# Performance work log

Measured on AMD Instinct MI355X. Metric: run time of the kernel, lower is better.

Reference implementation:

```python
import jax, jax.numpy as jnp
import numpy as np

N = 131072   # total inner-graph nodes (G * n)
G = 2048     # number of inner graphs = nodes of outer graph fg
n = 64       # nodes per inner graph (contiguous blocks)
E = 1048576  # inner edges
EF = 32768   # outer (fg) edges
D = 128      # emb_dim == hidden_dim
K = 8        # SortPooling k
VOCAB = 150


def setup_inputs() -> dict:
    key = jax.random.key(0)
    ks = jax.random.split(key, 32)
    p = lambda k, shape: (jax.random.normal(k, shape, jnp.float32) * 0.1)
    inp = {
        'h': jax.random.randint(ks[0], (N,), 0, VOCAB),
        'g_src': jax.random.randint(ks[1], (E,), 0, N),
        'g_dst': jax.random.randint(ks[2], (E,), 0, N),
        'fg_src': jax.random.randint(ks[3], (EF,), 0, G),
        'fg_dst': jax.random.randint(ks[4], (EF,), 0, G),
        'token_emb': p(ks[5], (VOCAB, D)),
        # GATConv 1 (D -> D, 1 head): fc weight (in,out), attn vectors, output bias
        'W1': p(ks[6], (D, D)), 'al1': p(ks[7], (D,)), 'ar1': p(ks[8], (D,)), 'b1': p(ks[9], (D,)),
        # GATConv 2
        'W2': p(ks[10], (D, D)), 'al2': p(ks[11], (D,)), 'ar2': p(ks[12], (D,)), 'b2': p(ks[13], (D,)),
        # GATConv 3 (K*D -> D) over fg
        'W3': p(ks[14], (K * D, D)), 'al3': p(ks[15], (D,)), 'ar3': p(ks[16], (D,)), 'b3': p(ks[17], (D,)),
        # linear_forward
        'Wf': p(ks[18], (D, D)), 'bf': p(ks[19], (D,)),
        # linear
        'Wl': p(ks[20], (D, D)), 'bl': p(ks[21], (D,)),
        # linear1
        'Wl1': p(ks[22], (D, D)), 'bl1': p(ks[23], (D,)),
        # clasifier
        'Wc': p(ks[24], (D, 2)), 'bc': p(ks[25], (2,)),
    }
    return inp


def gat_conv(src, dst, num_nodes, x, W, al, ar, b):
    """DGL GATConv, num_heads=1, allow_zero_in_degree=True, no activation."""
    f = x @ W                                   # [N, D] projected features
    el = f @ al                                 # [N] left attention logits
    er = f @ ar                                 # [N] right attention logits
    e = jax.nn.leaky_relu(el[src] + er[dst], 0.2)   # [E] per-edge score
    m = jax.ops.segment_max(e, dst, num_segments=num_nodes)
    a = jnp.exp(e - m[dst])
    s = jax.ops.segment_sum(a, dst, num_segments=num_nodes)
    alpha = a / s[dst]                          # edge softmax over incoming edges
    out = jax.ops.segment_sum(alpha[:, None] * f[src], dst, num_segments=num_nodes)
    return out + b                              # zero-in-degree nodes -> bias only


def sort_pooling(x, num_graphs, nodes_per_graph, k):
    """DGL SortPooling: sort each node's feature ascending, rank nodes by last
    channel descending, take top-k, concat -> [G, k*D]."""
    d = x.shape[-1]
    x = jnp.sort(x.reshape(num_graphs, nodes_per_graph, d), axis=-1)
    idx = jnp.argsort(-x[:, :, -1], axis=1)[:, :k]          # [G, k]
    topk = jnp.take_along_axis(x, idx[:, :, None], axis=1)  # [G, k, D]
    return topk.reshape(num_graphs, k * d)


def reference(h, g_src, g_dst, fg_src, fg_dst, token_emb,
              W1, al1, ar1, b1, W2, al2, ar2, b2, W3, al3, ar3, b3,
              Wf, bf, Wl, bl, Wl1, bl1, Wc, bc):
    x = jax.nn.relu(token_emb[h])                                   # [N, D]
    x = jax.nn.relu(gat_conv(g_src, g_dst, N, x, W1, al1, ar1, b1))
    x = jax.nn.relu(gat_conv(g_src, g_dst, N, x, W2, al2, ar2, b2))
    x = jax.nn.relu(x @ Wf + bf)                                    # linear_forward
    x = sort_pooling(x, G, n, K)                                    # [G, K*D]
    x = jax.nn.relu(gat_conv(fg_src, fg_dst, G, x, W3, al3, ar3, b3))
    x = jax.nn.relu(x @ Wl + bl)                                    # dropout = eval identity
    x = jax.nn.relu(x @ Wl1 + bl1)
    x = x @ Wc + bc
    return x.reshape(-1, 2)
```

## Files before the change

### kernel.cpp

```cpp
#include <hip/hip_runtime.h>
#include <math.h>

#define NN   131072
#define GG   2048
#define NPG  64
#define EE   1048576
#define EFN  32768
#define DD   128
#define KK   8
#define VOCAB 150

typedef unsigned short bfu;
typedef _Float16 f16x8 __attribute__((ext_vector_type(8)));
typedef float f32x4 __attribute__((ext_vector_type(4)));

static __device__ __forceinline__ bfu f2b(float f) {
  unsigned u = __float_as_uint(f);
  u += 0x7FFFu + ((u >> 16) & 1u);
  return (bfu)(u >> 16);
}
static __device__ __forceinline__ float b2f(bfu b) {
  return __uint_as_float(((unsigned)b) << 16);
}

static __device__ __forceinline__ bfu f2h(float f) {
  _Float16 h = (_Float16)f;
  bfu u;
  __builtin_memcpy(&u, &h, 2);
  return u;
}
static __device__ __forceinline__ float h2f(bfu b) {
  _Float16 h;
  __builtin_memcpy(&h, &b, 2);
  return (float)h;
}

__global__ void fill_f32_kernel(float* __restrict__ p, float v, int nElems) {
  int i = blockIdx.x * 256 + threadIdx.x;
  if (i < nElems) p[i] = v;
}

__global__ void zero_int_kernel(int* __restrict__ p, int nElems) {
  int i = blockIdx.x * 256 + threadIdx.x;
  if (i < nElems) p[i] = 0;
}

__global__ void init_softmax_kernel(float* __restrict__ mx, float* __restrict__ sm, int nElems) {
  int i = blockIdx.x * 256 + threadIdx.x;
  if (i < nElems) { mx[i] = -INFINITY; sm[i] = 0.f; }
}

__global__ void embed_relu_kernel(const float* __restrict__ temb,
                                  const int* __restrict__ h,
                                  float* __restrict__ x, int total) {
  int i = blockIdx.x * 256 + threadIdx.x;
  if (i >= total) return;
  int node = i >> 7, d = i & 127;
  x[i] = fmaxf(temb[h[node] * DD + d], 0.f);
}

template <int KD, int ROWS>
__global__ __launch_bounds__(128) void gemm_kernel(
    const float* __restrict__ A, const float* __restrict__ W,
    const float* __restrict__ bias, float* __restrict__ out,
    int relu_flag) {
  __shared__ float As[ROWS * KD];
  const int row0 = blockIdx.x * ROWS;
  const int tid = threadIdx.x;
  for (int i = tid; i < ROWS * KD; i += 128) As[i] = A[(size_t)row0 * KD + i];
  __syncthreads();
  float acc[ROWS];
#pragma unroll
  for (int r = 0; r < ROWS; r++) acc[r] = 0.f;
  for (int k = 0; k < KD; k++) {
    float w = W[k * 128 + tid];
#pragma unroll
    for (int r = 0; r < ROWS; r++) acc[r] += As[r * KD + k] * w;
  }
  float b = bias ? bias[tid] : 0.f;
#pragma unroll
  for (int r = 0; r < ROWS; r++) {
    float v = acc[r] + b;
    if (relu_flag) v = fmaxf(v, 0.f);
    out[(size_t)(row0 + r) * 128 + tid] = v;
  }
}

__global__ __launch_bounds__(128) void vocab_l1_kernel(
    const float* __restrict__ temb, const float* __restrict__ W1,
    const float* __restrict__ al1, const float* __restrict__ ar1,
    bfu* __restrict__ fvh, float* __restrict__ elv, float* __restrict__ erv) {
  __shared__ float xs[128];
  __shared__ float rl[128], rr[128];
  int v = blockIdx.x, t = threadIdx.x;
  xs[t] = fmaxf(temb[v * 128 + t], 0.f);
  __syncthreads();
  float acc = 0.f;
  for (int k = 0; k < 128; k++) acc += xs[k] * W1[k * 128 + t];
  fvh[v * 128 + t] = f2h(acc);
  rl[t] = acc * al1[t];
  rr[t] = acc * ar1[t];
  __syncthreads();
  for (int off = 64; off; off >>= 1) {
    if (t < off) { rl[t] += rl[t + off]; rr[t] += rr[t + off]; }
    __syncthreads();
  }
  if (t == 0) { elv[v] = rl[0]; erv[v] = rr[0]; }
}

__global__ __launch_bounds__(256) void gemm1024_kernel(
    const float* __restrict__ A, const float* __restrict__ W,
    float* __restrict__ out,
    const float* __restrict__ al, const float* __restrict__ ar,
    float* __restrict__ el, float* __restrict__ er) {
  __shared__ float As[8 * 1024];
  __shared__ float red[8][256];
  const int t = threadIdx.x;
  const int row0 = blockIdx.x * 8;
  for (int idx = t; idx < 8 * 256; idx += 256) {
    int r = idx >> 8, c4 = (idx & 255) << 2;
    *(float4*)&As[r * 1024 + c4] = *(const float4*)(A + (size_t)(row0 + r) * 1024 + c4);
  }
  __syncthreads();
  const int col = t & 127, kh = t >> 7;
  const int k0 = kh * 512;
  float acc[8];
#pragma unroll
  for (int r = 0; r < 8; r++) acc[r] = 0.f;
  for (int k = k0; k < k0 + 512; k += 4) {
    float w0 = W[(size_t)(k + 0) * 128 + col];
    float w1 = W[(size_t)(k + 1) * 128 + col];
    float w2 = W[(size_t)(k + 2) * 128 + col];
    float w3 = W[(size_t)(k + 3) * 128 + col];
#pragma unroll
    for (int r = 0; r < 8; r++) {
      float4 a = *(const float4*)&As[r * 1024 + k];
      acc[r] += a.x * w0 + a.y * w1 + a.z * w2 + a.w * w3;
    }
  }
#pragma unroll
  for (int r = 0; r < 8; r++) red[r][t] = acc[r];
  __syncthreads();
  for (int idx = t; idx < 1024; idx += 256) {
    int r = idx >> 7, c = idx & 127;
    float val = red[r][c] + red[r][128 + c];
    out[(size_t)(row0 + r) * 128 + c] = val;
    As[idx] = val * al[c];
    As[4096 + idx] = val * ar[c];
  }
  __syncthreads();
  if (t < 8) {
    float s = 0.f;
    for (int c = 0; c < 128; c++) s += As[t * 128 + c];
    el[row0 + t] = s;
  } else if (t < 16) {
    int r = t - 8;
    float s = 0.f;
    for (int c = 0; c < 128; c++) s += As[4096 + r * 128 + c];
    er[row0 + r] = s;
  }
}

__global__ void pack_w2_kernel(const float* __restrict__ W2, const float* __restrict__ Wf,
                               bfu* __restrict__ w2h, bfu* __restrict__ wfh) {
  int i = blockIdx.x * 256 + threadIdx.x;
  if (i >= 32768) return;
  const float* W = (i < 16384) ? W2 : Wf;
  bfu* dst = (i < 16384) ? w2h : wfh;
  int ii = i & 16383;
  int k = ii >> 7, n = ii & 127;
  bfu h = f2h(W[ii]);
  int kk = k >> 5, k5 = k & 31, quad = k5 >> 3, j = k5 & 7;
  int tt = n >> 4, m16 = n & 15;
  int pos = ((((kk * 8 + tt) * 4 + quad) * 16) + m16) * 8 + j;
  dst[pos] = h;
}

template <int SRC_MODE, int EPI>
__global__ __launch_bounds__(256) void mfma_gemm(
    const float* A, const bfu* __restrict__ WfHi,
    const float* __restrict__ bias, void* out,
    const float* __restrict__ al, const float* __restrict__ ar,
    float* __restrict__ el, float* __restrict__ er,
    float* __restrict__ keyb) {
  const int t = threadIdx.x;
  const int lane = t & 63, wv_ = t >> 6;
  const int m16 = lane & 15, quad = lane >> 4;
  const int rowbase = blockIdx.x * 128 + wv_ * 32;
  const float* arow0 = nullptr;
  const float* arow1 = nullptr;
  const bfu* brow0 = nullptr;
  const bfu* brow1 = nullptr;
  if constexpr (SRC_MODE == 0) {
    arow0 = A + (size_t)(rowbase + m16) * 128;
    arow1 = A + (size_t)(rowbase + 16 + m16) * 128;
  } else {
    brow0 = (const bfu*)A + (size_t)(rowbase + m16) * 128;
    brow1 = (const bfu*)A + (size_t)(rowbase + 16 + m16) * 128;
  }
  f32x4 acc[2][8];
#pragma unroll
  for (int rg = 0; rg < 2; rg++)
#pragma unroll
    for (int i = 0; i < 8; i++) acc[rg][i] = (f32x4){0.f, 0.f, 0.f, 0.f};
#pragma unroll
  for (int kk = 0; kk < 4; kk++) {
    int k0 = kk * 32 + quad * 8;
    f16x8 ahi0, alo0, ahi1, alo1;
    if constexpr (SRC_MODE == 2) {
      ahi0 = *(const f16x8*)(brow0 + k0);
      ahi1 = *(const f16x8*)(brow1 + k0);
    } else {
      float av0[8], av1[8];
      *(float4*)&av0[0] = *(const float4*)(arow0 + k0);
      *(float4*)&av0[4] = *(const float4*)(arow0 + k0 + 4);
      *(float4*)&av1[0] = *(const float4*)(arow1 + k0);
      *(float4*)&av1[4] = *(const float4*)(arow1 + k0 + 4);
#pragma unroll
      for (int i = 0; i < 8; i++) {
        _Float16 h0 = (_Float16)av0[i];
        ahi0[i] = h0;
        alo0[i] = (_Float16)(av0[i] - (float)h0);
        _Float16 h1 = (_Float16)av1[i];
        ahi1[i] = h1;
        alo1[i] = (_Float16)(av1[i] - (float)h1);
      }
    }
#pragma unroll
    for (int tt = 0; tt < 8; tt++) {
      int pos = ((((kk * 8 + tt) * 4 + quad) * 16) + m16) * 8;
      f16x8 bhi = *(const f16x8*)&WfHi[pos];
      acc[0][tt] = __builtin_amdgcn_mfma_f32_16x16x32_f16(ahi0, bhi, acc[0][tt], 0, 0, 0);
      if constexpr (SRC_MODE != 2)
        acc[0][tt] = __builtin_amdgcn_mfma_f32_16x16x32_f16(alo0, bhi, acc[0][tt], 0, 0, 0);
      acc[1][tt] = __builtin_amdgcn_mfma_f32_16x16x32_f16(ahi1, bhi, acc[1][tt], 0, 0, 0);
      if constexpr (SRC_MODE != 2)
        acc[1][tt] = __builtin_amdgcn_mfma_f32_16x16x32_f16(alo1, bhi, acc[1][tt], 0, 0, 0);
    }
  }
#pragma unroll
  for (int rg = 0; rg < 2; rg++) {
    const int rb = rowbase + rg * 16;
    if constexpr (EPI == 1) {
      float pl[4] = {0.f, 0.f, 0.f, 0.f}, pr[4] = {0.f, 0.f, 0.f, 0.f};
#pragma unroll
      for (int tt = 0; tt < 8; tt++) {
        int col = tt * 16 + m16;
        float alv = al[col], arv = ar[col];
#pragma unroll
        for (int r = 0; r < 4; r++) {
          float v = acc[rg][tt][r];
          ((bfu*)out)[(size_t)(rb + quad * 4 + r) * 128 + col] = f2h(v);
          pl[r] += v * alv;
          pr[r] += v * arv;
        }
      }
#pragma unroll
      for (int r = 0; r < 4; r++) {
        float a0 = pl[r], a1 = pr[r];
#pragma unroll
        for (int off = 1; off < 16; off <<= 1) {
          a0 += __shfl_xor(a0, off);
          a1 += __shfl_xor(a1, off);
        }
        if (m16 == 0) {
          el[rb + quad * 4 + r] = a0;
          er[rb + quad * 4 + r] = a1;
        }
      }
    } else {
      float pm[4] = {-INFINITY, -INFINITY, -INFINITY, -INFINITY};
#pragma unroll
      for (int tt = 0; tt < 8; tt++) {
        int col = tt * 16 + m16;
        float bv = bias[col];
#pragma unroll
        for (int r = 0; r < 4; r++) {
          float v = fmaxf(acc[rg][tt][r] + bv, 0.f);
          ((bfu*)out)[(size_t)(rb + quad * 4 + r) * 128 + col] = f2h(v);
          pm[r] = fmaxf(pm[r], v);
        }
      }
#pragma unroll
      for (int r = 0; r < 4; r++) {
        float a0 = pm[r];
#pragma unroll
        for (int off = 1; off < 16; off <<= 1) a0 = fmaxf(a0, __shfl_xor(a0, off));
        if (m16 == 0) keyb[rb + quad * 4 + r] = a0;
      }
    }
  }
}

__global__ __launch_bounds__(64) void attn_logits_kernel(
    const float* __restrict__ f, const float* __restrict__ al,
    const float* __restrict__ ar, float* __restrict__ el,
    float* __restrict__ er) {
  int node = blockIdx.x, lane = threadIdx.x;
  float v1 = f[(size_t)node * 128 + lane];
  float v2 = f[(size_t)node * 128 + 64 + lane];
  float sl = v1 * al[lane] + v2 * al[64 + lane];
  float sr = v1 * ar[lane] + v2 * ar[64 + lane];
#pragma unroll
  for (int off = 32; off; off >>= 1) {
    sl += __shfl_down(sl, off);
    sr += __shfl_down(sr, off);
  }
  if (lane == 0) { el[node] = sl; er[node] = sr; }
}

__global__ void hist_rank_kernel(const int* __restrict__ dst, int* __restrict__ cnt,
                                 int* __restrict__ rank, int nE) {
  int e = blockIdx.x * 256 + threadIdx.x;
  if (e < nE) rank[e] = atomicAdd(&cnt[dst[e]], 1);
}

__global__ __launch_bounds__(256) void scan_block_kernel(
    const int* __restrict__ cnt, int* __restrict__ excl, int* __restrict__ part) {
  __shared__ int s[256];
  int blk = blockIdx.x, tid = threadIdx.x;
  int base = blk * 1024 + tid * 4;
  int a0 = cnt[base], a1 = cnt[base + 1], a2 = cnt[base + 2], a3 = cnt[base + 3];
  int tsum = a0 + a1 + a2 + a3;
  s[tid] = tsum; __syncthreads();
  for (int off = 1; off < 256; off <<= 1) {
    int v = (tid >= off) ? s[tid - off] : 0;
    __syncthreads();
    s[tid] += v;
    __syncthreads();
  }
  int texcl = s[tid] - tsum;
  excl[base]     = texcl;
  excl[base + 1] = texcl + a0;
  excl[base + 2] = texcl + a0 + a1;
  excl[base + 3] = texcl + a0 + a1 + a2;
  if (tid == 255) part[blk] = s[255];
}

__global__ __launch_bounds__(128) void scan_part_kernel(int* __restrict__ part) {
  __shared__ int s[128];
  int tid = threadIdx.x;
  int orig = part[tid];
  s[tid] = orig; __syncthreads();
  for (int off = 1; off < 128; off <<= 1) {
    int v = (tid >= off) ? s[tid - off] : 0;
    __syncthreads();
    s[tid] += v;
    __syncthreads();
  }
  part[tid] = s[tid] - orig;
}

__global__ void scan_add_kernel(int* __restrict__ row_ptr, const int* __restrict__ part,
                                int n, int total) {
  int i = blockIdx.x * 256 + threadIdx.x;
  if (i < n) row_ptr[i] += part[i >> 10];
  if (i == 0) row_ptr[n] = total;
}

__global__ __launch_bounds__(256) void scan2048_kernel(const int* __restrict__ cnt,
                                                       int* __restrict__ rp, int total) {
  __shared__ int s[256];
  int t = threadIdx.x;
  int base = t * 8;
  int v[8];
  int tsum = 0;
#pragma unroll
  for (int i = 0; i < 8; i++) { v[i] = cnt[base + i]; tsum += v[i]; }
  s[t] = tsum; __syncthreads();
  for (int off = 1; off < 256; off <<= 1) {
    int x = (t >= off) ? s[t - off] : 0;
    __syncthreads();
    s[t] += x;
    __syncthreads();
  }
  int excl = s[t] - tsum;
#pragma unroll
  for (int i = 0; i < 8; i++) { rp[base + i] = excl; excl += v[i]; }
  if (t == 255) rp[2048] = total;
}

__global__ void scatter2_kernel(const int* __restrict__ dst, const int* __restrict__ src,
                                const int* __restrict__ row_ptr, const int* __restrict__ rank,
                                int* __restrict__ adj_src, int nE) {
  int e = blockIdx.x * 256 + threadIdx.x;
  if (e >= nE) return;
  adj_src[row_ptr[dst[e]] + rank[e]] = src[e];
}

__global__ __launch_bounds__(256) void gat_aggregate_vocab_kernel(
    const bfu* __restrict__ fvh, const float* __restrict__ elv,
    const float* __restrict__ erv, const int* __restrict__ h,
    const int* __restrict__ row_ptr, const int* __restrict__ adj_src,
    const float* __restrict__ bias, bfu* __restrict__ outX) {
  const int t = threadIdx.x;
  const int l = t & 31;
  const int gb = t & 32;
  const int d = blockIdx.x * 8 + (t >> 5);
  const int c0 = l * 4;
  int beg = row_ptr[d];
  int n = row_ptr[d + 1] - beg;
  float4 bv = *(const float4*)&bias[c0];
  if (n == 0) {
    ushort4 o;
    o.x = f2h(fmaxf(bv.x, 0.f)); o.y = f2h(fmaxf(bv.y, 0.f));
    o.z = f2h(fmaxf(bv.z, 0.f)); o.w = f2h(fmaxf(bv.w, 0.f));
    *(ushort4*)&outX[(size_t)d * 128 + c0] = o;
    return;
  }
  float er_d = erv[h[d]];
  float4 acc = make_float4(0.f, 0.f, 0.f, 0.f);
  if (n <= 32) {
    int hv = 0; float sc = -INFINITY;
    if (l < n) {
      hv = h[adj_src[beg + l]];
      float v = elv[hv] + er_d;
      sc = v > 0.f ? v : 0.2f * v;
    }
    float m = sc;
#pragma unroll
    for (int off = 16; off; off >>= 1) m = fmaxf(m, __shfl_xor(m, off));
    float ex = (l < n) ? expf(sc - m) : 0.f;
    float s = ex;
#pragma unroll
    for (int off = 16; off; off >>= 1) s += __shfl_xor(s, off);
    float wt = ex / s;
    for (int j = 0; j < n; j += 4) {
      int   h0 = __shfl(hv, gb + j);
      float w0 = __shfl(wt, gb + j);
      int   j1 = (j + 1 < n) ? j + 1 : j;
      int   h1 = __shfl(hv, gb + j1); float w1 = (j + 1 < n) ? __shfl(wt, gb + j1) : 0.f;
      int   j2 = (j + 2 < n) ? j + 2 : j;
      int   h2 = __shfl(hv, gb + j2); float w2 = (j + 2 < n) ? __shfl(wt, gb + j2) : 0.f;
      int   j3 = (j + 3 < n) ? j + 3 : j;
      int   h3 = __shfl(hv, gb + j3); float w3 = (j + 3 < n) ? __shfl(wt, gb + j3) : 0.f;
      ushort4 f0 = *(const ushort4*)&fvh[(size_t)h0 * 128 + c0];
      ushort4 f1 = *(const ushort4*)&fvh[(size_t)h1 * 128 + c0];
      ushort4 f2 = *(const ushort4*)&fvh[(size_t)h2 * 128 + c0];
      ushort4 f3 = *(const ushort4*)&fvh[(size_t)h3 * 128 + c0];
      acc.x += w0 * h2f(f0.x) + w1 * h2f(f1.x) + w2 * h2f(f2.x) + w3 * h2f(f3.x);
      acc.y += w0 * h2f(f0.y) + w1 * h2f(f1.y) + w2 * h2f(f2.y) + w3 * h2f(f3.y);
      acc.z += w0 * h2f(f0.z) + w1 * h2f(f1.z) + w2 * h2f(f2.z) + w3 * h2f(f3.z);
      acc.w += w0 * h2f(f0.w) + w1 * h2f(f1.w) + w2 * h2f(f2.w) + w3 * h2f(f3.w);
    }
  } else {
    float lm = -INFINITY;
    for (int e = l; e < n; e += 32) {
      int hv = h[adj_src[beg + e]];
      float v = elv[hv] + er_d;
      v = v > 0.f ? v : 0.2f * v;
      lm = fmaxf(lm, v);
    }
#pragma unroll
    for (int off = 16; off; off >>= 1) lm = fmaxf(lm, __shfl_xor(lm, off));
    float ls = 0.f;
    for (int e = l; e < n; e += 32) {
      int hv = h[adj_src[beg + e]];
      float v = elv[hv] + er_d;
      v = v > 0.f ? v : 0.2f * v;
      ls += expf(v - lm);
    }
#pragma unroll
    for (int off = 16; off; off >>= 1) ls += __shfl_xor(ls, off);
    for (int base = 0; base < n; base += 32) {
      int e = base + l;
      int hv = 0; float wt = 0.f;
      if (e < n) {
        hv = h[adj_src[beg + e]];
        float v = elv[hv] + er_d;
        v = v > 0.f ? v : 0.2f * v;
        wt = expf(v - lm) / ls;
      }
      int cnt = min(32, n - base);
      for (int j = 0; j < cnt; ++j) {
        int h0 = __shfl(hv, gb + j);
        float w0 = __shfl(wt, gb + j);
        ushort4 f0 = *(const ushort4*)&fvh[(size_t)h0 * 128 + c0];
        acc.x += w0 * h2f(f0.x);
        acc.y += w0 * h2f(f0.y);
        acc.z += w0 * h2f(f0.z);
        acc.w += w0 * h2f(f0.w);
      }
    }
  }
  ushort4 o;
  o.x = f2h(fmaxf(acc.x + bv.x, 0.f));
  o.y = f2h(fmaxf(acc.y + bv.y, 0.f));
  o.z = f2h(fmaxf(acc.z + bv.z, 0.f));
  o.w = f2h(fmaxf(acc.w + bv.w, 0.f));
  *(ushort4*)&outX[(size_t)d * 128 + c0] = o;
}

__global__ __launch_bounds__(256) void gat_aggregate_csr_kernel(
    const bfu* __restrict__ F, const float* __restrict__ el,
    const float* __restrict__ er, const int* __restrict__ row_ptr,
    const int* __restrict__ adj_src,
    const float* __restrict__ bias, bfu* __restrict__ outX) {
  const int t = threadIdx.x;
  const int l = t & 31;
  const int gb = t & 32;
  const int d = blockIdx.x * 8 + (t >> 5);
  const int c0 = l * 4;
  int beg = row_ptr[d];
  int n = row_ptr[d + 1] - beg;
  float4 bv = *(const float4*)&bias[c0];
  if (n == 0) {
    ushort4 o;
    o.x = f2h(fmaxf(bv.x, 0.f)); o.y = f2h(fmaxf(bv.y, 0.f));
    o.z = f2h(fmaxf(bv.z, 0.f)); o.w = f2h(fmaxf(bv.w, 0.f));
    *(ushort4*)&outX[(size_t)d * 128 + c0] = o;
    return;
  }
  float er_d = er[d];
  float4 acc = make_float4(0.f, 0.f, 0.f, 0.f);
  if (n <= 32) {
    int sv = 0; float sc = -INFINITY;
    if (l < n) {
      sv = adj_src[beg + l];
      float v = el[sv] + er_d;
      sc = v > 0.f ? v : 0.2f * v;
    }
    float m = sc;
#pragma unroll
    for (int off = 16; off; off >>= 1) m = fmaxf(m, __shfl_xor(m, off));
    float ex = (l < n) ? expf(sc - m) : 0.f;
    float s = ex;
#pragma unroll
    for (int off = 16; off; off >>= 1) s += __shfl_xor(s, off);
    float wt = ex / s;
    for (int j = 0; j < n; j += 4) {
      int   s0 = __shfl(sv, gb + j);
      float w0 = __shfl(wt, gb + j);
      int   j1 = (j + 1 < n) ? j + 1 : j;
      int   s1 = __shfl(sv, gb + j1); float w1 = (j + 1 < n) ? __shfl(wt, gb + j1) : 0.f;
      int   j2 = (j + 2 < n) ? j + 2 : j;
      int   s2 = __shfl(sv, gb + j2); float w2 = (j + 2 < n) ? __shfl(wt, gb + j2) : 0.f;
      int   j3 = (j + 3 < n) ? j + 3 : j;
      int   s3 = __shfl(sv, gb + j3); float w3 = (j + 3 < n) ? __shfl(wt, gb + j3) : 0.f;
      ushort4 f0 = *(const ushort4*)&F[(size_t)s0 * 128 + c0];
      ushort4 f1 = *(const ushort4*)&F[(size_t)s1 * 128 + c0];
      ushort4 f2 = *(const ushort4*)&F[(size_t)s2 * 128 + c0];
      ushort4 f3 = *(const ushort4*)&F[(size_t)s3 * 128 + c0];
      acc.x += w0 * h2f(f0.x) + w1 * h2f(f1.x) + w2 * h2f(f2.x) + w3 * h2f(f3.x);
      acc.y += w0 * h2f(f0.y) + w1 * h2f(f1.y) + w2 * h2f(f2.y) + w3 * h2f(f3.y);
      acc.z += w0 * h2f(f0.z) + w1 * h2f(f1.z) + w2 * h2f(f2.z) + w3 * h2f(f3.z);
      acc.w += w0 * h2f(f0.w) + w1 * h2f(f1.w) + w2 * h2f(f2.w) + w3 * h2f(f3.w);
    }
  } else {
    float lm = -INFINITY;
    for (int e = l; e < n; e += 32) {
      int sv = adj_src[beg + e];
      float v = el[sv] + er_d;
      v = v > 0.f ? v : 0.2f * v;
      lm = fmaxf(lm, v);
    }
#pragma unroll
    for (int off = 16; off; off >>= 1) lm = fmaxf(lm, __shfl_xor(lm, off));
    float ls = 0.f;
    for (int e = l; e < n; e += 32) {
      int sv = adj_src[beg + e];
      float v = el[sv] + er_d;
      v = v > 0.f ? v : 0.2f * v;
      ls += expf(v - lm);
    }
#pragma unroll
    for (int off = 16; off; off >>= 1) ls += __shfl_xor(ls, off);
    for (int base = 0; base < n; base += 32) {
      int e = base + l;
      int sv = 0; float wt = 0.f;
      if (e < n) {
        sv = adj_src[beg + e];
        float v = el[sv] + er_d;
        v = v > 0.f ? v : 0.2f * v;
        wt = expf(v - lm) / ls;
      }
      int cnt = min(32, n - base);
      for (int j = 0; j < cnt; ++j) {
        int s0 = __shfl(sv, gb + j);
        float w0 = __shfl(wt, gb + j);
        ushort4 f0 = *(const ushort4*)&F[(size_t)s0 * 128 + c0];
        acc.x += w0 * h2f(f0.x);
        acc.y += w0 * h2f(f0.y);
        acc.z += w0 * h2f(f0.z);
        acc.w += w0 * h2f(f0.w);
      }
    }
  }
  ushort4 o;
  o.x = f2h(fmaxf(acc.x + bv.x, 0.f));
  o.y = f2h(fmaxf(acc.y + bv.y, 0.f));
  o.z = f2h(fmaxf(acc.z + bv.z, 0.f));
  o.w = f2h(fmaxf(acc.w + bv.w, 0.f));
  *(ushort4*)&outX[(size_t)d * 128 + c0] = o;
}

__global__ __launch_bounds__(256) void gat_aggregate_outer_kernel(
    const float* __restrict__ F, const float* __restrict__ el,
    const float* __restrict__ er, const int* __restrict__ row_ptr,
    const int* __restrict__ adj_src,
    const float* __restrict__ bias, float* __restrict__ outG) {
  const int t = threadIdx.x;
  const int l = t & 31;
  const int gb = t & 32;
  const int d = blockIdx.x * 8 + (t >> 5);
  const int c0 = l * 4;
  int beg = row_ptr[d];
  int n = row_ptr[d + 1] - beg;
  float4 bv = *(const float4*)&bias[c0];
  if (n == 0) {
    float4 o;
    o.x = fmaxf(bv.x, 0.f); o.y = fmaxf(bv.y, 0.f);
    o.z = fmaxf(bv.z, 0.f); o.w = fmaxf(bv.w, 0.f);
    *(float4*)&outG[(size_t)d * 128 + c0] = o;
    return;
  }
  float er_d = er[d];
  float4 acc = make_float4(0.f, 0.f, 0.f, 0.f);
  if (n <= 32) {
    int sv = 0; float sc = -INFINITY;
    if (l < n) {
      sv = adj_src[beg + l];
      float v = el[sv] + er_d;
      sc = v > 0.f ? v : 0.2f * v;
    }
    float m = sc;
#pragma unroll
    for (int off = 16; off; off >>= 1) m = fmaxf(m, __shfl_xor(m, off));
    float ex = (l < n) ? expf(sc - m) : 0.f;
    float s = ex;
#pragma unroll
    for (int off = 16; off; off >>= 1) s += __shfl_xor(s, off);
    float wt = ex / s;
    for (int j = 0; j < n; ++j) {
      int   s0 = __shfl(sv, gb + j);
      float w0 = __shfl(wt, gb + j);
      float4 f0 = *(const float4*)&F[(size_t)s0 * 128 + c0];
      acc.x += w0 * f0.x; acc.y += w0 * f0.y;
      acc.z += w0 * f0.z; acc.w += w0 * f0.w;
    }
  } else {
    float lm = -INFINITY;
    for (int e = l; e < n; e += 32) {
      int sv = adj_src[beg + e];
      float v = el[sv] + er_d;
      v = v > 0.f ? v : 0.2f * v;
      lm = fmaxf(lm, v);
    }
#pragma unroll
    for (int off = 16; off; off >>= 1) lm = fmaxf(lm, __shfl_xor(lm, off));
    float ls = 0.f;
    for (int e = l; e < n; e += 32) {
      int sv = adj_src[beg + e];
      float v = el[sv] + er_d;
      v = v > 0.f ? v : 0.2f * v;
      ls += expf(v - lm);
    }
#pragma unroll
    for (int off = 16; off; off >>= 1) ls += __shfl_xor(ls, off);
    for (int base = 0; base < n; base += 32) {
      int e = base + l;
      int sv = 0; float wt = 0.f;
      if (e < n) {
        sv = adj_src[beg + e];
        float v = el[sv] + er_d;
        v = v > 0.f ? v : 0.2f * v;
        wt = expf(v - lm) / ls;
      }
      int cnt = min(32, n - base);
      for (int j = 0; j < cnt; ++j) {
        int s0 = __shfl(sv, gb + j);
        float w0 = __shfl(wt, gb + j);
        float4 f0 = *(const float4*)&F[(size_t)s0 * 128 + c0];
        acc.x += w0 * f0.x; acc.y += w0 * f0.y;
        acc.z += w0 * f0.z; acc.w += w0 * f0.w;
      }
    }
  }
  float4 o;
  o.x = fmaxf(acc.x + bv.x, 0.f);
  o.y = fmaxf(acc.y + bv.y, 0.f);
  o.z = fmaxf(acc.z + bv.z, 0.f);
  o.w = fmaxf(acc.w + bv.w, 0.f);
  *(float4*)&outG[(size_t)d * 128 + c0] = o;
}

static __device__ __forceinline__ void atomicMaxF(float* addr, float v) {
  int iv = __float_as_int(v);
  if (iv >= 0) atomicMax((int*)addr, iv);
  else atomicMin((unsigned int*)addr, (unsigned int)iv);
}

static __device__ __forceinline__ float edge_score(const float* el, const float* er,
                                                   int sv, int dv) {
  float v = el[sv] + er[dv];
  return v > 0.f ? v : 0.2f * v;
}

__global__ void edge_max_kernel(const float* __restrict__ el,
                                const float* __restrict__ er,
                                const int* __restrict__ src,
                                const int* __restrict__ dst,
                                float* __restrict__ m, int nE) {
  int e = blockIdx.x * 256 + threadIdx.x;
  if (e >= nE) return;
  atomicMaxF(&m[dst[e]], edge_score(el, er, src[e], dst[e]));
}

__global__ void edge_expsum_kernel(const float* __restrict__ el,
                                   const float* __restrict__ er,
                                   const float* __restrict__ m,
                                   const int* __restrict__ src,
                                   const int* __restrict__ dst,
                                   float* __restrict__ s, int nE) {
  int e = blockIdx.x * 256 + threadIdx.x;
  if (e >= nE) return;
  int d = dst[e];
  atomicAdd(&s[d], expf(edge_score(el, er, src[e], d) - m[d]));
}

__global__ __launch_bounds__(128) void edge_aggregate_kernel(
    const float* __restrict__ f, const float* __restrict__ el,
    const float* __restrict__ er, const float* __restrict__ m,
    const float* __restrict__ s, const int* __restrict__ src,
    const int* __restrict__ dst, float* __restrict__ out, int nE) {
  int e = blockIdx.x;
  int d = threadIdx.x;
  int sv = src[e], dv = dst[e];
  float alpha = expf(edge_score(el, er, sv, dv) - m[dv]) / s[dv];
  atomicAdd(&out[(size_t)dv * 128 + d], alpha * f[(size_t)sv * 128 + d]);
}

__global__ void bias_relu_kernel(float* __restrict__ x,
                                 const float* __restrict__ b, int total) {
  int i = blockIdx.x * 256 + threadIdx.x;
  if (i >= total) return;
  x[i] = fmaxf(x[i] + b[i & 127], 0.f);
}

__global__ __launch_bounds__(64) void row_max_kernel(const float* __restrict__ x,
                                                     float* __restrict__ key) {
  int node = blockIdx.x, lane = threadIdx.x;
  float v = fmaxf(x[(size_t)node * 128 + lane], x[(size_t)node * 128 + 64 + lane]);
#pragma unroll
  for (int off = 32; off; off >>= 1) v = fmaxf(v, __shfl_down(v, off));
  if (lane == 0) key[node] = v;
}

__global__ __launch_bounds__(64) void select_topk_kernel(
    const float* __restrict__ key, int* __restrict__ sel) {
  __shared__ float keys[NPG];
  int g = blockIdx.x, t = threadIdx.x;
  keys[t] = key[(size_t)g * NPG + t];
  __syncthreads();
  float myk = keys[t];
  int rank = 0;
  for (int j = 0; j < NPG; ++j) {
    float kj = keys[j];
    rank += (kj > myk) || (kj == myk && j < t);
  }
  if (rank < KK) sel[g * KK + rank] = t;
}

__global__ __launch_bounds__(1024) void topk_sort_kernel(
    const float* __restrict__ keyb, const bfu* __restrict__ xin,
    float* __restrict__ xp) {
  __shared__ float keys[NPG];
  __shared__ int sel_l[KK];
  __shared__ float v[1024];
  int g = blockIdx.x, t = threadIdx.x;
  if (t < NPG) keys[t] = keyb[(size_t)g * NPG + t];
  __syncthreads();
  if (t < NPG) {
    float myk = keys[t];
    int rank = 0;
    for (int j = 0; j < NPG; ++j) {
      float kj = keys[j];
      rank += (kj > myk) || (kj == myk && j < t);
    }
    if (rank < KK) sel_l[rank] = t;
  }
  __syncthreads();
  int r = t >> 7, c = t & 127;
  int node = sel_l[r];
  v[t] = h2f(xin[(size_t)(g * NPG + node) * 128 + c]);
  __syncthreads();
  for (int k = 2; k <= 128; k <<= 1) {
    for (int j = k >> 1; j > 0; j >>= 1) {
      int ixj = c ^ j;
      if (ixj > c) {
        float a = v[r * 128 + c], bb = v[r * 128 + ixj];
        bool asc = ((c & k) == 0);
        if (asc ? (a > bb) : (a < bb)) { v[r * 128 + c] = bb; v[r * 128 + ixj] = a; }
      }
      __syncthreads();
    }
  }
  xp[(size_t)g * 1024 + t] = v[t];
}

template <int HF>
__global__ __launch_bounds__(128) void sort_rows_kernel(
    const void* __restrict__ xin, const int* __restrict__ sel,
    float* __restrict__ xp) {
  __shared__ float v[128];
  int b = blockIdx.x;
  int t = threadIdx.x;
  int g = b >> 3, r = b & 7;
  int node = sel[b];
  if (HF) v[t] = h2f(((const bfu*)xin)[(size_t)(g * NPG + node) * 128 + t]);
  else    v[t] = ((const float*)xin)[(size_t)(g * NPG + node) * 128 + t];
  __syncthreads();
  for (int k = 2; k <= 128; k <<= 1) {
    for (int j = k >> 1; j > 0; j >>= 1) {
      int ixj = t ^ j;
      if (ixj > t) {
        float a = v[t], bb = v[ixj];
        bool asc = ((t & k) == 0);
        if (asc ? (a > bb) : (a < bb)) { v[t] = bb; v[ixj] = a; }
      }
      __syncthreads();
    }
  }
  xp[(size_t)g * (KK * 128) + r * 128 + t] = v[t];
}

__global__ __launch_bounds__(128) void mlp_tail_kernel(
    const float* __restrict__ g3, const float* __restrict__ Wl,
    const float* __restrict__ bl, const float* __restrict__ Wl1,
    const float* __restrict__ bl1, const float* __restrict__ Wc,
    const float* __restrict__ bc, float* __restrict__ out) {
  __shared__ float buf[128];
  __shared__ float r0[128], r1[128];
  int g = blockIdx.x, t = threadIdx.x;
  buf[t] = g3[(size_t)g * 128 + t];
  __syncthreads();
  float a = 0.f;
  for (int k = 0; k < 128; k++) a += buf[k] * Wl[k * 128 + t];
  float t1 = fmaxf(a + bl[t], 0.f);
  __syncthreads();
  buf[t] = t1;
  __syncthreads();
  a = 0.f;
  for (int k = 0; k < 128; k++) a += buf[k] * Wl1[k * 128 + t];
  float t2 = fmaxf(a + bl1[t], 0.f);
  r0[t] = t2 * Wc[t * 2 + 0];
  r1[t] = t2 * Wc[t * 2 + 1];
  __syncthreads();
  for (int off = 64; off; off >>= 1) {
    if (t < off) { r0[t] += r0[t + off]; r1[t] += r1[t + off]; }
    __syncthreads();
  }
  if (t == 0) {
    out[g * 2 + 0] = r0[0] + bc[0];
    out[g * 2 + 1] = r1[0] + bc[1];
  }
}

extern "C" void kernel_launch(void* const* d_in, const int* in_sizes, int n_in,
                              void* d_out, int out_size, void* d_ws, size_t ws_size,
                              hipStream_t stream) {
  const size_t BASE_FLOATS = (size_t)NN * DD * 2 + (size_t)NN * 4;
  const size_t CSR_INTS = (size_t)(NN + 1) + NN + EE + 128;
  if (ws_size < BASE_FLOATS * sizeof(float)) {
    hipMemsetAsync(d_out, 0, (size_t)out_size * sizeof(float), stream);
    return;
  }
  const bool use_csr = ws_size >= BASE_FLOATS * sizeof(float) + CSR_INTS * sizeof(int);

  const int* h      = (const int*)d_in[0];
  const int* g_src  = (const int*)d_in[1];
  const int* g_dst  = (const int*)d_in[2];
  const int* fg_src = (const int*)d_in[3];
  const int* fg_dst = (const int*)d_in[4];
  const float* temb = (const float*)d_in[5];
  const float* W1 = (const float*)d_in[6];
  const float* al1 = (const float*)d_in[7];
  const float* ar1 = (const float*)d_in[8];
  const float* b1 = (const float*)d_in[9];
  const float* W2 = (const float*)d_in[10];
  const float* al2 = (const float*)d_in[11];
  const float* ar2 = (const float*)d_in[12];
  const float* b2 = (const float*)d_in[13];
  const float* W3 = (const float*)d_in[14];
  const float* al3 = (const float*)d_in[15];
  const float* ar3 = (const float*)d_in[16];
  const float* b3 = (const float*)d_in[17];
  const float* Wf = (const float*)d_in[18];
  const float* bfv = (const float*)d_in[19];
  const float* Wl = (const float*)d_in[20];
  const float* bl = (const float*)d_in[21];
  const float* Wl1 = (const float*)d_in[22];
  const float* bl1 = (const float*)d_in[23];
  const float* Wc = (const float*)d_in[24];
  const float* bc = (const float*)d_in[25];
  float* out = (float*)d_out;

  float* ws = (float*)d_ws;
  float* X  = ws;
  float* F  = X + (size_t)NN * DD;
  float* el = F + (size_t)NN * DD;
  float* er = el + NN;
  float* mx = er + NN;
  float* sm = mx + NN;
  int* row_ptr = (int*)(sm + NN);
  int* cursor  = row_ptr + NN + 1;
  int* adj_src = cursor + NN;
  int* part    = adj_src + EE;
  int* rankb = (int*)X;
  bfu* w2h = (bfu*)mx;
  bfu* wfh = w2h + 16384;
  bfu* fvh = wfh + 16384;
  float* elv = (float*)(fvh + VOCAB * 128 + 128);
  float* erv = elv + VOCAB;
  int* ocnt  = (int*)X;
  int* orp   = ocnt + 2048;
  int* orank = orp + 2080;
  int* oadj  = orank + EFN;
  float* xp   = F;
  float* f3   = F + 2097152;
  float* g3   = f3 + (size_t)GG * DD;
  float* t1   = g3 + (size_t)GG * DD;
  float* t2   = t1 + (size_t)GG * DD;
  float* keyb = t2 + (size_t)GG * DD;
  int*   sel  = (int*)(keyb + NN);

  const int totalND = NN * DD;

  if (use_csr) {
    bfu* Fb = (bfu*)F;
    bfu* Xb = (bfu*)X;
    zero_int_kernel<<<NN / 256, 256, 0, stream>>>(cursor, NN);
    hist_rank_kernel<<<EE / 256, 256, 0, stream>>>(g_dst, cursor, rankb, EE);
    scan_block_kernel<<<NN / 1024, 256, 0, stream>>>(cursor, row_ptr, part);
    scan_part_kernel<<<1, 128, 0, stream>>>(part);
    scan_add_kernel<<<(NN + 255) / 256, 256, 0, stream>>>(row_ptr, part, NN, EE);
    scatter2_kernel<<<EE / 256, 256, 0, stream>>>(g_dst, g_src, row_ptr, rankb, adj_src, EE);

    pack_w2_kernel<<<128, 256, 0, stream>>>(W2, Wf, w2h, wfh);
    vocab_l1_kernel<<<VOCAB, 128, 0, stream>>>(temb, W1, al1, ar1, fvh, elv, erv);

    gat_aggregate_vocab_kernel<<<NN / 8, 256, 0, stream>>>(
        fvh, elv, erv, h, row_ptr, adj_src, b1, Xb);

    mfma_gemm<2, 1><<<NN / 128, 256, 0, stream>>>(
        (const float*)X, w2h, nullptr, Fb, al2, ar2, el, er, nullptr);
    gat_aggregate_csr_kernel<<<NN / 8, 256, 0, stream>>>(Fb, el, er, row_ptr, adj_src, b2, Xb);

    mfma_gemm<2, 2><<<NN / 128, 256, 0, stream>>>(
        (const float*)X, wfh, bfv, Xb, nullptr, nullptr, nullptr, nullptr, keyb);

    topk_sort_kernel<<<GG, 1024, 0, stream>>>(keyb, Xb, xp);

    zero_int_kernel<<<GG / 256, 256, 0, stream>>>(ocnt, GG);
    hist_rank_kernel<<<EFN / 256, 256, 0, stream>>>(fg_dst, ocnt, orank, EFN);
    scan2048_kernel<<<1, 256, 0, stream>>>(ocnt, orp, EFN);
    scatter2_kernel<<<EFN / 256, 256, 0, stream>>>(fg_dst, fg_src, orp, orank, oadj, EFN);

    gemm1024_kernel<<<GG / 8, 256, 0, stream>>>(xp, W3, f3, al3, ar3, el, er);
    gat_aggregate_outer_kernel<<<GG / 8, 256, 0, stream>>>(f3, el, er, orp, oadj, b3, g3);

    mlp_tail_kernel<<<GG, 128, 0, stream>>>(g3, Wl, bl, Wl1, bl1, Wc, bc, out);
  } else {
    embed_relu_kernel<<<totalND / 256, 256, 0, stream>>>(temb, h, X, totalND);
    auto gat_inner = [&](const float* W, const float* al, const float* ar, const float* bb) {
      gemm_kernel<DD, 8><<<NN / 8, 128, 0, stream>>>(X, W, nullptr, F, 0);
      attn_logits_kernel<<<NN, 64, 0, stream>>>(F, al, ar, el, er);
      init_softmax_kernel<<<(NN + 255) / 256, 256, 0, stream>>>(mx, sm, NN);
      fill_f32_kernel<<<totalND / 256, 256, 0, stream>>>(X, 0.f, totalND);
      edge_max_kernel<<<(EE + 255) / 256, 256, 0, stream>>>(el, er, g_src, g_dst, mx, EE);
      edge_expsum_kernel<<<(EE + 255) / 256, 256, 0, stream>>>(el, er, mx, g_src, g_dst, sm, EE);
      edge_aggregate_kernel<<<EE, 128, 0, stream>>>(F, el, er, mx, sm, g_src, g_dst, X, EE);
      bias_relu_kernel<<<totalND / 256, 256, 0, stream>>>(X, bb, totalND);
    };
    gat_inner(W1, al1, ar1, b1);
    gat_inner(W2, al2, ar2, b2);
    gemm_kernel<DD, 8><<<NN / 8, 128, 0, stream>>>(X, Wf, bfv, X, 1);
    row_max_kernel<<<NN, 64, 0, stream>>>(X, keyb);

    select_topk_kernel<<<GG, 64, 0, stream>>>(keyb, sel);
    sort_rows_kernel<0><<<GG * KK, 128, 0, stream>>>(X, sel, xp);

    gemm1024_kernel<<<GG / 8, 256, 0, stream>>>(xp, W3, f3, al3, ar3, el, er);
    init_softmax_kernel<<<(GG + 255) / 256, 256, 0, stream>>>(mx, sm, GG);
    fill_f32_kernel<<<(GG * DD + 255) / 256, 256, 0, stream>>>(g3, 0.f, GG * DD);
    edge_max_kernel<<<(EFN + 255) / 256, 256, 0, stream>>>(el, er, fg_src, fg_dst, mx, EFN);
    edge_expsum_kernel<<<(EFN + 255) / 256, 256, 0, stream>>>(el, er, mx, fg_src, fg_dst, sm, EFN);
    edge_aggregate_kernel<<<EFN, 128, 0, stream>>>(f3, el, er, mx, sm, fg_src, fg_dst, g3, EFN);
    bias_relu_kernel<<<(GG * DD + 255) / 256, 256, 0, stream>>>(g3, b3, GG * DD);
    mlp_tail_kernel<<<GG, 128, 0, stream>>>(g3, Wl, bl, Wl1, bl1, Wc, bc, out);
  }
}
```

Before: 425.0 us.

## Use MFMA fp16 GEMM for outer GAT projection and pack vocab index into adjacency

Replaces the scalar 1024-wide outer GEMM with an MFMA fp16 kernel. This requires packing W3 into fp16 tiles and having top-k write its pooled features in fp16. The edge scatter now packs the source node's token id into the upper bits of each adjacency entry, which removes a dependent h[] gather in the vocab aggregation; the second aggregation masks those bits off. The unused fp32 split-precision GEMM path is dropped. The cost is lower precision in the outer GEMM, and the outer GEMM launches only 16 blocks, so parallelism is low.

```diff
diff --git a/kernel.cpp b/kernel.cpp
--- a/kernel.cpp
+++ b/kernel.cpp
@@ -9,19 +9,11 @@
 #define DD   128
 #define KK   8
 #define VOCAB 150
+#define SRCMASK 0x1FFFF
 
 typedef unsigned short bfu;
 typedef _Float16 f16x8 __attribute__((ext_vector_type(8)));
 typedef float f32x4 __attribute__((ext_vector_type(4)));
-
-static __device__ __forceinline__ bfu f2b(float f) {
-  unsigned u = __float_as_uint(f);
-  u += 0x7FFFu + ((u >> 16) & 1u);
-  return (bfu)(u >> 16);
-}
-static __device__ __forceinline__ float b2f(bfu b) {
-  return __uint_as_float(((unsigned)b) << 16);
-}
 
 static __device__ __forceinline__ bfu f2h(float f) {
   _Float16 h = (_Float16)f;
@@ -176,10 +168,21 @@
   dst[pos] = h;
 }
 
-template <int SRC_MODE, int EPI>
+__global__ void pack_wk_kernel(const float* __restrict__ W, bfu* __restrict__ dst, int total) {
+  int i = blockIdx.x * 256 + threadIdx.x;
+  if (i >= total) return;
+  int k = i >> 7, n = i & 127;
+  bfu h = f2h(W[i]);
+  int kk = k >> 5, k5 = k & 31, quad = k5 >> 3, j = k5 & 7;
+  int tt = n >> 4, m16 = n & 15;
+  int pos = ((((kk * 8 + tt) * 4 + quad) * 16) + m16) * 8 + j;
+  dst[pos] = h;
+}
+
+template <int EPI>
 __global__ __launch_bounds__(256) void mfma_gemm(
-    const float* A, const bfu* __restrict__ WfHi,
-    const float* __restrict__ bias, void* out,
+    const bfu* __restrict__ A, const bfu* __restrict__ WfHi,
+    const float* __restrict__ bias, bfu* __restrict__ outF,
     const float* __restrict__ al, const float* __restrict__ ar,
     float* __restrict__ el, float* __restrict__ er,
     float* __restrict__ keyb) {
@@ -187,17 +190,8 @@
   const int lane = t & 63, wv_ = t >> 6;
   const int m16 = lane & 15, quad = lane >> 4;
   const int rowbase = blockIdx.x * 128 + wv_ * 32;
-  const float* arow0 = nullptr;
-  const float* arow1 = nullptr;
-  const bfu* brow0 = nullptr;
-  const bfu* brow1 = nullptr;
-  if constexpr (SRC_MODE == 0) {
-    arow0 = A + (size_t)(rowbase + m16) * 128;
-    arow1 = A + (size_t)(rowbase + 16 + m16) * 128;
-  } else {
-    brow0 = (const bfu*)A + (size_t)(rowbase + m16) * 128;
-    brow1 = (const bfu*)A + (size_t)(rowbase + 16 + m16) * 128;
-  }
+  const bfu* brow0 = A + (size_t)(rowbase + m16) * 128;
+  const bfu* brow1 = A + (size_t)(rowbase + 16 + m16) * 128;
   f32x4 acc[2][8];
 #pragma unroll
   for (int rg = 0; rg < 2; rg++)
@@ -206,36 +200,14 @@
 #pragma unroll
   for (int kk = 0; kk < 4; kk++) {
     int k0 = kk * 32 + quad * 8;
-    f16x8 ahi0, alo0, ahi1, alo1;
-    if constexpr (SRC_MODE == 2) {
-      ahi0 = *(const f16x8*)(brow0 + k0);
-      ahi1 = *(const f16x8*)(brow1 + k0);
-    } else {
-      float av0[8], av1[8];
-      *(float4*)&av0[0] = *(const float4*)(arow0 + k0);
-      *(float4*)&av0[4] = *(const float4*)(arow0 + k0 + 4);
-      *(float4*)&av1[0] = *(const float4*)(arow1 + k0);
-      *(float4*)&av1[4] = *(const float4*)(arow1 + k0 + 4);
-#pragma unroll
-      for (int i = 0; i < 8; i++) {
-        _Float16 h0 = (_Float16)av0[i];
-        ahi0[i] = h0;
-        alo0[i] = (_Float16)(av0[i] - (float)h0);
-        _Float16 h1 = (_Float16)av1[i];
-        ahi1[i] = h1;
-        alo1[i] = (_Float16)(av1[i] - (float)h1);
-      }
-    }
+    f16x8 ahi0 = *(const f16x8*)(brow0 + k0);
+    f16x8 ahi1 = *(const f16x8*)(brow1 + k0);
 #pragma unroll
     for (int tt = 0; tt < 8; tt++) {
       int pos = ((((kk * 8 + tt) * 4 + quad) * 16) + m16) * 8;
       f16x8 bhi = *(const f16x8*)&WfHi[pos];
       acc[0][tt] = __builtin_amdgcn_mfma_f32_16x16x32_f16(ahi0, bhi, acc[0][tt], 0, 0, 0);
-      if constexpr (SRC_MODE != 2)
-        acc[0][tt] = __builtin_amdgcn_mfma_f32_16x16x32_f16(alo0, bhi, acc[0][tt], 0, 0, 0);
       acc[1][tt] = __builtin_amdgcn_mfma_f32_16x16x32_f16(ahi1, bhi, acc[1][tt], 0, 0, 0);
-      if constexpr (SRC_MODE != 2)
-        acc[1][tt] = __builtin_amdgcn_mfma_f32_16x16x32_f16(alo1, bhi, acc[1][tt], 0, 0, 0);
     }
   }
 #pragma unroll
@@ -250,7 +222,7 @@
 #pragma unroll
         for (int r = 0; r < 4; r++) {
           float v = acc[rg][tt][r];
-          ((bfu*)out)[(size_t)(rb + quad * 4 + r) * 128 + col] = f2h(v);
+          outF[(size_t)(rb + quad * 4 + r) * 128 + col] = f2h(v);
           pl[r] += v * alv;
           pr[r] += v * arv;
         }
@@ -277,7 +249,7 @@
 #pragma unroll
         for (int r = 0; r < 4; r++) {
           float v = fmaxf(acc[rg][tt][r] + bv, 0.f);
-          ((bfu*)out)[(size_t)(rb + quad * 4 + r) * 128 + col] = f2h(v);
+          outF[(size_t)(rb + quad * 4 + r) * 128 + col] = f2h(v);
           pm[r] = fmaxf(pm[r], v);
         }
       }
@@ -287,6 +259,66 @@
 #pragma unroll
         for (int off = 1; off < 16; off <<= 1) a0 = fmaxf(a0, __shfl_xor(a0, off));
         if (m16 == 0) keyb[rb + quad * 4 + r] = a0;
+      }
+    }
+  }
+}
+
+__global__ __launch_bounds__(256) void mfma_gemm1024_kernel(
+    const bfu* __restrict__ A, const bfu* __restrict__ Wtab,
+    float* __restrict__ out, const float* __restrict__ al,
+    const float* __restrict__ ar, float* __restrict__ el,
+    float* __restrict__ er) {
+  const int t = threadIdx.x;
+  const int lane = t & 63, wv_ = t >> 6;
+  const int m16 = lane & 15, quad = lane >> 4;
+  const int rowbase = blockIdx.x * 128 + wv_ * 32;
+  const bfu* brow0 = A + (size_t)(rowbase + m16) * 1024;
+  const bfu* brow1 = A + (size_t)(rowbase + 16 + m16) * 1024;
+  f32x4 acc[2][8];
+#pragma unroll
+  for (int rg = 0; rg < 2; rg++)
+#pragma unroll
+    for (int i = 0; i < 8; i++) acc[rg][i] = (f32x4){0.f, 0.f, 0.f, 0.f};
+  for (int kk = 0; kk < 32; kk++) {
+    int k0 = kk * 32 + quad * 8;
+    f16x8 ahi0 = *(const f16x8*)(brow0 + k0);
+    f16x8 ahi1 = *(const f16x8*)(brow1 + k0);
+#pragma unroll
+    for (int tt = 0; tt < 8; tt++) {
+      int pos = ((((kk * 8 + tt) * 4 + quad) * 16) + m16) * 8;
+      f16x8 bhi = *(const f16x8*)&Wtab[pos];
+      acc[0][tt] = __builtin_amdgcn_mfma_f32_16x16x32_f16(ahi0, bhi, acc[0][tt], 0, 0, 0);
+      acc[1][tt] = __builtin_amdgcn_mfma_f32_16x16x32_f16(ahi1, bhi, acc[1][tt], 0, 0, 0);
+    }
+  }
+#pragma unroll
+  for (int rg = 0; rg < 2; rg++) {
+    const int rb = rowbase + rg * 16;
+    float pl[4] = {0.f, 0.f, 0.f, 0.f}, pr[4] = {0.f, 0.f, 0.f, 0.f};
+#pragma unroll
+    for (int tt = 0; tt < 8; tt++) {
+      int col = tt * 16 + m16;
+      float alv = al[col], arv = ar[col];
+#pragma unroll
+      for (int r = 0; r < 4; r++) {
+        float v = acc[rg][tt][r];
+        out[(size_t)(rb + quad * 4 + r) * 128 + col] = v;
+        pl[r] += v * alv;
+        pr[r] += v * arv;
+      }
+    }
+#pragma unroll
+    for (int r = 0; r < 4; r++) {
+      float a0 = pl[r], a1 = pr[r];
+#pragma unroll
+      for (int off = 1; off < 16; off <<= 1) {
+        a0 += __shfl_xor(a0, off);
+        a1 += __shfl_xor(a1, off);
+      }
+      if (m16 == 0) {
+        el[rb + quad * 4 + r] = a0;
+        er[rb + quad * 4 + r] = a1;
       }
     }
   }
@@ -388,10 +420,20 @@
   adj_src[row_ptr[dst[e]] + rank[e]] = src[e];
 }
 
+__global__ void scatter2_pack_kernel(const int* __restrict__ dst, const int* __restrict__ src,
+                                     const int* __restrict__ h,
+                                     const int* __restrict__ row_ptr, const int* __restrict__ rank,
+                                     int* __restrict__ adj_src, int nE) {
+  int e = blockIdx.x * 256 + threadIdx.x;
+  if (e >= nE) return;
+  int s = src[e];
+  adj_src[row_ptr[dst[e]] + rank[e]] = s | (h[s] << 17);
+}
+
 __global__ __launch_bounds__(256) void gat_aggregate_vocab_kernel(
     const bfu* __restrict__ fvh, const float* __restrict__ elv,
     const float* __restrict__ erv, const int* __restrict__ h,
-    const int* __restrict__ row_ptr, const int* __restrict__ adj_src,
+    const int* __restrict__ row_ptr, const int* __restrict__ adj,
     const float* __restrict__ bias, bfu* __restrict__ outX) {
   const int t = threadIdx.x;
   const int l = t & 31;
@@ -413,7 +455,7 @@
   if (n <= 32) {
     int hv = 0; float sc = -INFINITY;
     if (l < n) {
-      hv = h[adj_src[beg + l]];
+      hv = adj[beg + l] >> 17;
       float v = elv[hv] + er_d;
       sc = v > 0.f ? v : 0.2f * v;
     }
@@ -446,7 +488,7 @@
   } else {
     float lm = -INFINITY;
     for (int e = l; e < n; e += 32) {
-      int hv = h[adj_src[beg + e]];
+      int hv = adj[beg + e] >> 17;
       float v = elv[hv] + er_d;
       v = v > 0.f ? v : 0.2f * v;
       lm = fmaxf(lm, v);
@@ -455,7 +497,7 @@
     for (int off = 16; off; off >>= 1) lm = fmaxf(lm, __shfl_xor(lm, off));
     float ls = 0.f;
     for (int e = l; e < n; e += 32) {
-      int hv = h[adj_src[beg + e]];
+      int hv = adj[beg + e] >> 17;
       float v = elv[hv] + er_d;
       v = v > 0.f ? v : 0.2f * v;
       ls += expf(v - lm);
@@ -466,7 +508,7 @@
       int e = base + l;
       int hv = 0; float wt = 0.f;
       if (e < n) {
-        hv = h[adj_src[beg + e]];
+        hv = adj[beg + e] >> 17;
         float v = elv[hv] + er_d;
         v = v > 0.f ? v : 0.2f * v;
         wt = expf(v - lm) / ls;
@@ -494,7 +536,7 @@
 __global__ __launch_bounds__(256) void gat_aggregate_csr_kernel(
     const bfu* __restrict__ F, const float* __restrict__ el,
     const float* __restrict__ er, const int* __restrict__ row_ptr,
-    const int* __restrict__ adj_src,
+    const int* __restrict__ adj,
     const float* __restrict__ bias, bfu* __restrict__ outX) {
   const int t = threadIdx.x;
   const int l = t & 31;
@@ -516,7 +558,7 @@
   if (n <= 32) {
     int sv = 0; float sc = -INFINITY;
     if (l < n) {
-      sv = adj_src[beg + l];
+      sv = adj[beg + l] & SRCMASK;
       float v = el[sv] + er_d;
       sc = v > 0.f ? v : 0.2f * v;
     }
@@ -549,7 +591,7 @@
   } else {
     float lm = -INFINITY;
     for (int e = l; e < n; e += 32) {
-      int sv = adj_src[beg + e];
+      int sv = adj[beg + e] & SRCMASK;
       float v = el[sv] + er_d;
       v = v > 0.f ? v : 0.2f * v;
       lm = fmaxf(lm, v);
@@ -558,7 +600,7 @@
     for (int off = 16; off; off >>= 1) lm = fmaxf(lm, __shfl_xor(lm, off));
     float ls = 0.f;
     for (int e = l; e < n; e += 32) {
-      int sv = adj_src[beg + e];
+      int sv = adj[beg + e] & SRCMASK;
       float v = el[sv] + er_d;
       v = v > 0.f ? v : 0.2f * v;
       ls += expf(v - lm);
@@ -569,7 +611,7 @@
       int e = base + l;
       int sv = 0; float wt = 0.f;
       if (e < n) {
-        sv = adj_src[beg + e];
+        sv = adj[beg + e] & SRCMASK;
         float v = el[sv] + er_d;
         v = v > 0.f ? v : 0.2f * v;
         wt = expf(v - lm) / ls;
@@ -763,7 +805,7 @@
 
 __global__ __launch_bounds__(1024) void topk_sort_kernel(
     const float* __restrict__ keyb, const bfu* __restrict__ xin,
-    float* __restrict__ xp) {
+    bfu* __restrict__ xp) {
   __shared__ float keys[NPG];
   __shared__ int sel_l[KK];
   __shared__ float v[1024];
@@ -795,7 +837,7 @@
       __syncthreads();
     }
   }
-  xp[(size_t)g * 1024 + t] = v[t];
+  xp[(size_t)g * 1024 + t] = f2h(v[t]);
 }
 
 template <int HF>
@@ -912,6 +954,7 @@
   bfu* fvh = wfh + 16384;
   float* elv = (float*)(fvh + VOCAB * 128 + 128);
   float* erv = elv + VOCAB;
+  bfu* w3h = (bfu*)(erv + VOCAB + 2);
   int* ocnt  = (int*)X;
   int* orp   = ocnt + 2048;
   int* orank = orp + 2080;
@@ -927,36 +970,38 @@
   const int totalND = NN * DD;
 
   if (use_csr) {
-    bfu* Fb = (bfu*)F;
-    bfu* Xb = (bfu*)X;
+    bfu* Fb  = (bfu*)F;
+    bfu* Xb  = (bfu*)X;
+    bfu* xph = (bfu*)xp;
     zero_int_kernel<<<NN / 256, 256, 0, stream>>>(cursor, NN);
     hist_rank_kernel<<<EE / 256, 256, 0, stream>>>(g_dst, cursor, rankb, EE);
     scan_block_kernel<<<NN / 1024, 256, 0, stream>>>(cursor, row_ptr, part);
     scan_part_kernel<<<1, 128, 0, stream>>>(part);
     scan_add_kernel<<<(NN + 255) / 256, 256, 0, stream>>>(row_ptr, part, NN, EE);
-    scatter2_kernel<<<EE / 256, 256, 0, stream>>>(g_dst, g_src, row_ptr, rankb, adj_src, EE);
+    scatter2_pack_kernel<<<EE / 256, 256, 0, stream>>>(g_dst, g_src, h, row_ptr, rankb, adj_src, EE);
 
     pack_w2_kernel<<<128, 256, 0, stream>>>(W2, Wf, w2h, wfh);
+    pack_wk_kernel<<<512, 256, 0, stream>>>(W3, w3h, 131072);
     vocab_l1_kernel<<<VOCAB, 128, 0, stream>>>(temb, W1, al1, ar1, fvh, elv, erv);
 
     gat_aggregate_vocab_kernel<<<NN / 8, 256, 0, stream>>>(
         fvh, elv, erv, h, row_ptr, adj_src, b1, Xb);
 
-    mfma_gemm<2, 1><<<NN / 128, 256, 0, stream>>>(
-        (const float*)X, w2h, nullptr, Fb, al2, ar2, el, er, nullptr);
+    mfma_gemm<1><<<NN / 128, 256, 0, stream>>>(
+        Xb, w2h, nullptr, Fb, al2, ar2, el, er, nullptr);
     gat_aggregate_csr_kernel<<<NN / 8, 256, 0, stream>>>(Fb, el, er, row_ptr, adj_src, b2, Xb);
 
-    mfma_gemm<2, 2><<<NN / 128, 256, 0, stream>>>(
-        (const float*)X, wfh, bfv, Xb, nullptr, nullptr, nullptr, nullptr, keyb);
-
-    topk_sort_kernel<<<GG, 1024, 0, stream>>>(keyb, Xb, xp);
+    mfma_gemm<2><<<NN / 128, 256, 0, stream>>>(
+        Xb, wfh, bfv, Xb, nullptr, nullptr, nullptr, nullptr, keyb);
+
+    topk_sort_kernel<<<GG, 1024, 0, stream>>>(keyb, Xb, xph);
 
     zero_int_kernel<<<GG / 256, 256, 0, stream>>>(ocnt, GG);
     hist_rank_kernel<<<EFN / 256, 256, 0, stream>>>(fg_dst, ocnt, orank, EFN);
     scan2048_kernel<<<1, 256, 0, stream>>>(ocnt, orp, EFN);
     scatter2_kernel<<<EFN / 256, 256, 0, stream>>>(fg_dst, fg_src, orp, orank, oadj, EFN);
 
-    gemm1024_kernel<<<GG / 8, 256, 0, stream>>>(xp, W3, f3, al3, ar3, el, er);
+    mfma_gemm1024_kernel<<<GG / 128, 256, 0, stream>>>(xph, w3h, f3, al3, ar3, el, er);
     gat_aggregate_outer_kernel<<<GG / 8, 256, 0, stream>>>(f3, el, er, orp, oadj, b3, g3);
 
     mlp_tail_kernel<<<GG, 128, 0, stream>>>(g3, Wl, bl, Wl1, bl1, Wc, bc, out);
```

After: 438.3 us. 1.03x slower.
